# Kernel optimization log

Measured on AMD Instinct MI355X. Metric: run time of the kernel, lower is better.

Reference implementation:

```python
import jax, jax.numpy as jnp
import numpy as np

D_MODEL = 512
N_HEADS = 8
D_HEAD = D_MODEL // N_HEADS
SCALE = 1.0 / np.sqrt(D_MODEL).astype(np.float32)  # source divides by sqrt(d_model), not sqrt(d_head)


def setup_inputs() -> dict:
    key = jax.random.key(0)
    ks = jax.random.split(key, 9)
    B, S = 4, 2048
    std = 1.0 / np.sqrt(D_MODEL).astype(np.float32)
    x = jax.random.normal(ks[0], (B, S, D_MODEL), dtype=jnp.float32)
    Wq = jax.random.normal(ks[1], (D_MODEL, D_MODEL), dtype=jnp.float32) * std
    bq = jnp.zeros((D_MODEL,), jnp.float32)
    Wk = jax.random.normal(ks[2], (D_MODEL, D_MODEL), dtype=jnp.float32) * std
    bk = jnp.zeros((D_MODEL,), jnp.float32)
    Wv = jax.random.normal(ks[3], (D_MODEL, D_MODEL), dtype=jnp.float32) * std
    bv = jnp.zeros((D_MODEL,), jnp.float32)
    Wo = jax.random.normal(ks[4], (D_MODEL, D_MODEL), dtype=jnp.float32) * std
    bo = jnp.zeros((D_MODEL,), jnp.float32)
    return {"x": x, "Wq": Wq, "bq": bq, "Wk": Wk, "bk": bk,
            "Wv": Wv, "bv": bv, "Wo": Wo, "bo": bo}


def reference(x, Wq, bq, Wk, bk, Wv, bv, Wo, bo):
    B, S, _ = x.shape
    # projections -> [B, H, S, Dh]
    def split_heads(t):
        return t.reshape(B, S, N_HEADS, D_HEAD).transpose(0, 2, 1, 3)
    q = split_heads(x @ Wq + bq)
    k = split_heads(x @ Wk + bk)
    v = split_heads(x @ Wv + bv)
    # scores: [B, H, S, S], scaled by 1/sqrt(d_model) as in source
    scores = jnp.einsum('bhqd,bhkd->bhqk', q, k) * SCALE
    weights = jax.nn.softmax(scores, axis=-1)
    # dropout is identity at inference time
    att = jnp.einsum('bhqk,bhkd->bhqd', weights, v)
    att = att.transpose(0, 2, 1, 3).reshape(B, S, D_MODEL)
    return att @ Wo + bo
```

## Files before the change

kernel.cpp:

```cpp
#include <hip/hip_runtime.h>
#include <math.h>

#define BATCH   4
#define S_LEN   2048
#define DMODEL  512
#define NHEADS  8
#define DHEAD   64
#define M_TOT   8192
#define ATT_SCALE 0.04419417382415922f
#define QSCALE (ATT_SCALE * 1.44269504088896f)

using short8  = __attribute__((ext_vector_type(8))) short;
using short4v = __attribute__((ext_vector_type(4))) short;
using floatx4 = __attribute__((ext_vector_type(4))) float;

__device__ __forceinline__ ushort f2bf(float f) {
    union { float f; unsigned u; } x; x.f = f;
    unsigned u = x.u + 0x7FFFu + ((x.u >> 16) & 1u);
    return (ushort)(u >> 16);
}
__device__ __forceinline__ unsigned pk2(float a, float b) {
    return (unsigned)f2bf(a) | ((unsigned)f2bf(b) << 16);
}
__device__ __forceinline__ unsigned pkr2(float a, float b) {
    unsigned ua = __float_as_uint(a) + 0x8000u;
    unsigned ub = __float_as_uint(b) + 0x8000u;
    return __builtin_amdgcn_perm(ub, ua, 0x07060302u);
}

__global__ __launch_bounds__(256) void prep(
    const float* __restrict__ x,
    const float* __restrict__ Wq, const float* __restrict__ Wk,
    const float* __restrict__ Wv, const float* __restrict__ Wo,
    ushort* __restrict__ xb, ushort* __restrict__ WT)
{
    const int bid = blockIdx.x;
    if (bid < 4096) {
        const int i = (bid * 256 + threadIdx.x) * 4;
        float4 f = *(const float4*)(x + i);
        uint2 o; o.x = pk2(f.x, f.y); o.y = pk2(f.z, f.w);
        *(uint2*)(xb + i) = o;
    } else {
        const int rb = bid - 4096;
        const int p  = rb >> 6;
        const int rem = rb & 63;
        const int n  = (rem >> 5) * 256 + threadIdx.x;
        const int k0 = (rem & 31) * 16;
        const float* W = (p == 0) ? Wq : (p == 1) ? Wk : (p == 2) ? Wv : Wo;
        unsigned u[8];
        #pragma unroll
        for (int j = 0; j < 8; ++j) {
            float a = W[(k0 + 2 * j)     * DMODEL + n];
            float b = W[(k0 + 2 * j + 1) * DMODEL + n];
            u[j] = pk2(a, b);
        }
        ushort* dst = WT + ((size_t)p * DMODEL + n) * DMODEL + k0;
        *(uint4*)dst       = *(uint4*)&u[0];
        *(uint4*)(dst + 8) = *(uint4*)&u[4];
    }
}

__global__ __launch_bounds__(256, 4) void qkv_gemm(
    const ushort* __restrict__ xb, const ushort* __restrict__ WT,
    const float* __restrict__ bq, const float* __restrict__ bk, const float* __restrict__ bv,
    ushort* __restrict__ q, ushort* __restrict__ k, ushort* __restrict__ vT)
{
    __shared__ ushort SMEM[128 * 136];
    ushort (*A)[40] = (ushort(*)[40])SMEM;
    ushort (*B)[40] = (ushort(*)[40])(SMEM + 128 * 40);
    ushort (*CT)[136] = (ushort(*)[136])SMEM;

    const int tid = threadIdx.x;
    const int wv  = tid >> 6, lane = tid & 63, l16 = lane & 15, quad = lane >> 4;
    const int m0  = blockIdx.x * 128;
    const int ng0 = blockIdx.y * 128;
    const int p   = ng0 >> 9;
    const int n0  = ng0 & 511;
    const ushort* Wp  = WT + (size_t)p * DMODEL * DMODEL + (size_t)n0 * DMODEL;
    const float* bias = (p == 0) ? bq : (p == 1) ? bk : bv;
    const float scl   = (p == 0) ? QSCALE : 1.0f;

    const int wm = (wv & 1) * 64, wn = (wv >> 1) * 64;
    floatx4 acc[4][4] = {};
    const int ar = tid >> 1, ac = (tid & 1) * 16;

    uint4 pa0, pa1, pb0, pb1;
    pa0 = *(const uint4*)(xb + (size_t)(m0 + ar) * DMODEL + ac);
    pa1 = *(const uint4*)(xb + (size_t)(m0 + ar) * DMODEL + ac + 8);
    pb0 = *(const uint4*)(Wp + (size_t)ar * DMODEL + ac);
    pb1 = *(const uint4*)(Wp + (size_t)ar * DMODEL + ac + 8);

    for (int k0 = 0; k0 < DMODEL; k0 += 32) {
        *(uint4*)&A[ar][ac] = pa0; *(uint4*)&A[ar][ac + 8] = pa1;
        *(uint4*)&B[ar][ac] = pb0; *(uint4*)&B[ar][ac + 8] = pb1;
        __syncthreads();

        if (k0 + 32 < DMODEL) {
            pa0 = *(const uint4*)(xb + (size_t)(m0 + ar) * DMODEL + k0 + 32 + ac);
            pa1 = *(const uint4*)(xb + (size_t)(m0 + ar) * DMODEL + k0 + 32 + ac + 8);
            pb0 = *(const uint4*)(Wp + (size_t)ar * DMODEL + k0 + 32 + ac);
            pb1 = *(const uint4*)(Wp + (size_t)ar * DMODEL + k0 + 32 + ac + 8);
        }

        short8 af[4], bf[4];
        #pragma unroll
        for (int i = 0; i < 4; ++i) af[i] = *(const short8*)&A[wm + i * 16 + l16][quad * 8];
        #pragma unroll
        for (int c = 0; c < 4; ++c) bf[c] = *(const short8*)&B[wn + c * 16 + l16][quad * 8];
        #pragma unroll
        for (int i = 0; i < 4; ++i)
            #pragma unroll
            for (int c = 0; c < 4; ++c)
                acc[i][c] = __builtin_amdgcn_mfma_f32_16x16x32_bf16(af[i], bf[c], acc[i][c], 0, 0, 0);
        __syncthreads();
    }

    if (p < 2) {
        #pragma unroll
        for (int c = 0; c < 4; ++c) {
            const int n = n0 + wn + c * 16 + l16;
            const float bb = bias[n];
            const int h = n >> 6, dh = n & 63;
            #pragma unroll
            for (int i = 0; i < 4; ++i)
                #pragma unroll
                for (int r = 0; r < 4; ++r) {
                    const int m = m0 + wm + i * 16 + quad * 4 + r;
                    const int b = m >> 11, s = m & 2047;
                    const ushort val = f2bf((acc[i][c][r] + bb) * scl);
                    if (p == 0) q[((size_t)(b * NHEADS + h) * S_LEN + s) * DHEAD + dh] = val;
                    else        k[((size_t)(b * NHEADS + h) * S_LEN + s) * DHEAD + dh] = val;
                }
        }
    } else {
        #pragma unroll
        for (int c = 0; c < 4; ++c) {
            const int n = wn + c * 16 + l16;
            const float bb = bias[n0 + n];
            #pragma unroll
            for (int i = 0; i < 4; ++i) {
                uint2 o;
                o.x = pk2(acc[i][c][0] + bb, acc[i][c][1] + bb);
                o.y = pk2(acc[i][c][2] + bb, acc[i][c][3] + bb);
                *(uint2*)&CT[n][wm + i * 16 + quad * 4] = o;
            }
        }
        __syncthreads();
        const int n  = tid >> 1, mh = (tid & 1) * 64;
        const int gn = n0 + n;
        const int h  = gn >> 6, dh = gn & 63;
        const int b  = m0 >> 11, sb = (m0 & 2047) + mh;
        ushort* dst = vT + ((size_t)(b * NHEADS + h) * DHEAD + dh) * S_LEN + sb;
        #pragma unroll
        for (int j = 0; j < 8; ++j)
            *(uint4*)(dst + j * 8) = *(const uint4*)&CT[n][mh + j * 8];
    }
}

__global__ __launch_bounds__(256, 4) void attn(
    const ushort* __restrict__ Q, const ushort* __restrict__ K,
    const ushort* __restrict__ vT,
    ushort* __restrict__ att, const int KT)
{
    __shared__ ushort Klds[2][64][72];
    __shared__ ushort Vt[2][64][72];

    const int tid = threadIdx.x;
    const int wv  = tid >> 6, lane = tid & 63, l16 = lane & 15, quad = lane >> 4;
    const int q0  = blockIdx.x * 128;
    const int bh  = blockIdx.y;
    const ushort* Qh = Q  + (size_t)bh * S_LEN * DHEAD;
    const ushort* Kh = K  + (size_t)bh * S_LEN * DHEAD;
    const ushort* Vh = vT + (size_t)bh * DHEAD * S_LEN;

    short8 qf[2][2];
    #pragma unroll
    for (int ni = 0; ni < 2; ++ni) {
        const ushort* qrow = Qh + (size_t)(q0 + wv * 32 + ni * 16 + l16) * DHEAD;
        qf[0][ni] = *(const short8*)(qrow + quad * 8);
        qf[1][ni] = *(const short8*)(qrow + 32 + quad * 8);
    }

    floatx4 oacc[4][2] = {};
    float lsum[2] = {0.f, 0.f};

    const int srow = tid >> 2, sc0 = (tid & 3) * 16;
    uint4 ka, kb, va, vb;
    {
        const ushort* Ks = Kh + (size_t)srow * DHEAD + sc0;
        const ushort* Vs = Vh + (size_t)srow * S_LEN + sc0;
        ka = *(const uint4*)Ks; kb = *(const uint4*)(Ks + 8);
        va = *(const uint4*)Vs; vb = *(const uint4*)(Vs + 8);
    }

    for (int kt = 0; kt < KT; ++kt) {
        const int buf = kt & 1;
        *(uint4*)&Klds[buf][srow][sc0] = ka; *(uint4*)&Klds[buf][srow][sc0 + 8] = kb;
        *(uint4*)&Vt[buf][srow][sc0]   = va; *(uint4*)&Vt[buf][srow][sc0 + 8]   = vb;
        __syncthreads();

        if (kt + 1 < KT) {
            const ushort* Ks = Kh + (size_t)((kt + 1) * 64 + srow) * DHEAD + sc0;
            const ushort* Vs = Vh + (size_t)srow * S_LEN + (kt + 1) * 64 + sc0;
            ka = *(const uint4*)Ks; kb = *(const uint4*)(Ks + 8);
            va = *(const uint4*)Vs; vb = *(const uint4*)(Vs + 8);
        }

        #pragma unroll
        for (int mi = 0; mi < 4; ++mi) {
            floatx4 s0 = {}, s1 = {};
            #pragma unroll
            for (int s = 0; s < 2; ++s) {
                short8 kf = *(const short8*)&Klds[buf][mi * 16 + l16][s * 32 + quad * 8];
                s0 = __builtin_amdgcn_mfma_f32_16x16x32_bf16(kf, qf[s][0], s0, 0, 0, 0);
                s1 = __builtin_amdgcn_mfma_f32_16x16x32_bf16(kf, qf[s][1], s1, 0, 0, 0);
            }
            short4v vfr[4];
            #pragma unroll
            for (int c = 0; c < 4; ++c)
                vfr[c] = *(const short4v*)&Vt[buf][c * 16 + l16][mi * 16 + quad * 4];

            {
                const float p0 = __builtin_amdgcn_exp2f(s0[0]);
                const float p1 = __builtin_amdgcn_exp2f(s0[1]);
                const float p2 = __builtin_amdgcn_exp2f(s0[2]);
                const float p3 = __builtin_amdgcn_exp2f(s0[3]);
                lsum[0] += (p0 + p1) + (p2 + p3);
                uint2 o; o.x = pkr2(p0, p1); o.y = pkr2(p2, p3);
                short4v pf; *(uint2*)&pf = o;
                #pragma unroll
                for (int c = 0; c < 4; ++c)
                    oacc[c][0] = __builtin_amdgcn_mfma_f32_16x16x16bf16_1k(vfr[c], pf, oacc[c][0], 0, 0, 0);
            }
            {
                const float p0 = __builtin_amdgcn_exp2f(s1[0]);
                const float p1 = __builtin_amdgcn_exp2f(s1[1]);
                const float p2 = __builtin_amdgcn_exp2f(s1[2]);
                const float p3 = __builtin_amdgcn_exp2f(s1[3]);
                lsum[1] += (p0 + p1) + (p2 + p3);
                uint2 o; o.x = pkr2(p0, p1); o.y = pkr2(p2, p3);
                short4v pf; *(uint2*)&pf = o;
                #pragma unroll
                for (int c = 0; c < 4; ++c)
                    oacc[c][1] = __builtin_amdgcn_mfma_f32_16x16x16bf16_1k(vfr[c], pf, oacc[c][1], 0, 0, 0);
            }
        }
    }

    float rin[2];
    #pragma unroll
    for (int ni = 0; ni < 2; ++ni) {
        float t = lsum[ni];
        t += __shfl_xor(t, 16, 64);
        t += __shfl_xor(t, 32, 64);
        rin[ni] = 1.0f / t;
    }

    const int b = bh >> 3, h = bh & 7;
    #pragma unroll
    for (int ni = 0; ni < 2; ++ni) {
        const int qg = q0 + wv * 32 + ni * 16 + l16;
        ushort* orow = att + ((size_t)(b * S_LEN + qg)) * DMODEL + h * DHEAD + quad * 4;
        #pragma unroll
        for (int c = 0; c < 4; ++c) {
            uint2 o;
            o.x = pk2(oacc[c][ni][0] * rin[ni], oacc[c][ni][1] * rin[ni]);
            o.y = pk2(oacc[c][ni][2] * rin[ni], oacc[c][ni][3] * rin[ni]);
            *(uint2*)(orow + c * 16) = o;
        }
    }
}

__global__ __launch_bounds__(256, 4) void out_gemm(
    const ushort* __restrict__ att,
    const ushort* __restrict__ WoT, const float* __restrict__ bo,
    float* __restrict__ out)
{
    __shared__ ushort A[64][40];
    __shared__ ushort B[128][40];

    const int tid = threadIdx.x;
    const int wv  = tid >> 6, lane = tid & 63, l16 = lane & 15, quad = lane >> 4;
    const int m0 = blockIdx.x * 64;
    const int n0 = blockIdx.y * 128;

    const int ar = tid >> 2, ac = (tid & 3) * 8;
    const int br = tid >> 1, bc = (tid & 1) * 16;

    floatx4 acc[8] = {};

    for (int k0 = 0; k0 < DMODEL; k0 += 32) {
        *(uint4*)&A[ar][ac] = *(const uint4*)(att + (size_t)(m0 + ar) * DMODEL + k0 + ac);
        uint4 b0 = *(const uint4*)(WoT + (size_t)(n0 + br) * DMODEL + k0 + bc);
        uint4 b1 = *(const uint4*)(WoT + (size_t)(n0 + br) * DMODEL + k0 + bc + 8);
        *(uint4*)&B[br][bc] = b0; *(uint4*)&B[br][bc + 8] = b1;
        __syncthreads();

        short8 af = *(const short8*)&A[wv * 16 + l16][quad * 8];
        #pragma unroll
        for (int c = 0; c < 8; ++c) {
            short8 bf = *(const short8*)&B[c * 16 + l16][quad * 8];
            acc[c] = __builtin_amdgcn_mfma_f32_16x16x32_bf16(af, bf, acc[c], 0, 0, 0);
        }
        __syncthreads();
    }

    #pragma unroll
    for (int c = 0; c < 8; ++c) {
        const int n = n0 + c * 16 + l16;
        const float bb = bo[n];
        #pragma unroll
        for (int r = 0; r < 4; ++r) {
            const int m = m0 + wv * 16 + quad * 4 + r;
            out[(size_t)m * DMODEL + n] = acc[c][r] + bb;
        }
    }
}

extern "C" void kernel_launch(void* const* d_in, const int* in_sizes, int n_in,
                              void* d_out, int out_size, void* d_ws, size_t ws_size,
                              hipStream_t stream)
{
    const float* x  = (const float*)d_in[0];
    const float* Wq = (const float*)d_in[1];
    const float* bq = (const float*)d_in[2];
    const float* Wk = (const float*)d_in[3];
    const float* bk = (const float*)d_in[4];
    const float* Wv = (const float*)d_in[5];
    const float* bv = (const float*)d_in[6];
    const float* Wo = (const float*)d_in[7];
    const float* bo = (const float*)d_in[8];
    float* out = (float*)d_out;

    ushort* ws = (ushort*)d_ws;
    const size_t SZ = (size_t)M_TOT * DMODEL;
    ushort* xb  = ws;
    ushort* WT  = ws + SZ;
    ushort* q   = WT + 4 * (size_t)DMODEL * DMODEL;
    ushort* k   = q + SZ;
    ushort* vT  = k + SZ;
    ushort* att = vT + SZ;

    prep<<<4096 + 256, 256, 0, stream>>>(x, Wq, Wk, Wv, Wo, xb, WT);

    qkv_gemm<<<dim3(M_TOT / 128, 3 * DMODEL / 128), 256, 0, stream>>>(
        xb, WT, bq, bk, bv, q, k, vT);

    attn<<<dim3(S_LEN / 128, BATCH * NHEADS), 256, 0, stream>>>(
        q, k, vT, att, S_LEN / 64);

    out_gemm<<<dim3(M_TOT / 64, DMODEL / 128), 256, 0, stream>>>(
        att, WT + 3 * (size_t)DMODEL * DMODEL, bo, out);
}
```

Baseline: 174.2 us.

## Split key tiles across wave halves in attention and prefetch out-GEMM tiles

The attention kernel now uses 512-thread blocks covering 256 queries. Each wave handles 64 queries and half of each 64-key tile, so every K fragment loaded from LDS feeds four query sub-tiles instead of two, with s_setprio hints around the MFMA bursts. The two key-half partial outputs and row sums are combined through LDS at the end, which adds extra synchronisation and a reduction. The output GEMM also register-prefetches the next K-slice of A and B while computing the current one. The larger per-wave accumulator state raises register pressure, and the attention grid has half as many blocks.

```diff
diff --git a/kernel.cpp b/kernel.cpp
--- a/kernel.cpp
+++ b/kernel.cpp
@@ -157,117 +157,149 @@
     }
 }
 
-__global__ __launch_bounds__(256, 4) void attn(
+__global__ __launch_bounds__(512, 2) void attn(
     const ushort* __restrict__ Q, const ushort* __restrict__ K,
     const ushort* __restrict__ vT,
     ushort* __restrict__ att, const int KT)
 {
-    __shared__ ushort Klds[2][64][72];
-    __shared__ ushort Vt[2][64][72];
-
-    const int tid = threadIdx.x;
-    const int wv  = tid >> 6, lane = tid & 63, l16 = lane & 15, quad = lane >> 4;
-    const int q0  = blockIdx.x * 128;
-    const int bh  = blockIdx.y;
+    __shared__ ushort SMEM[18432];
+    ushort (*Klds)[64][72] = (ushort(*)[64][72])SMEM;
+    ushort (*Vt)[64][72]   = (ushort(*)[64][72])(SMEM + 9216);
+    float  (*Ored)[68]     = (float(*)[68])SMEM;
+    float*  Lred           = (float*)SMEM + 128 * 68;
+
+    const int tid  = threadIdx.x;
+    const int wv   = tid >> 6, lane = tid & 63, l16 = lane & 15, quad = lane >> 4;
+    const int qsub = wv & 3, khalf = wv >> 2;
+    const int q0   = blockIdx.x * 256;
+    const int bh   = blockIdx.y;
     const ushort* Qh = Q  + (size_t)bh * S_LEN * DHEAD;
     const ushort* Kh = K  + (size_t)bh * S_LEN * DHEAD;
     const ushort* Vh = vT + (size_t)bh * DHEAD * S_LEN;
 
-    short8 qf[2][2];
-    #pragma unroll
-    for (int ni = 0; ni < 2; ++ni) {
-        const ushort* qrow = Qh + (size_t)(q0 + wv * 32 + ni * 16 + l16) * DHEAD;
+    short8 qf[2][4];
+    #pragma unroll
+    for (int ni = 0; ni < 4; ++ni) {
+        const ushort* qrow = Qh + (size_t)(q0 + qsub * 64 + ni * 16 + l16) * DHEAD;
         qf[0][ni] = *(const short8*)(qrow + quad * 8);
         qf[1][ni] = *(const short8*)(qrow + 32 + quad * 8);
     }
 
-    floatx4 oacc[4][2] = {};
-    float lsum[2] = {0.f, 0.f};
-
-    const int srow = tid >> 2, sc0 = (tid & 3) * 16;
-    uint4 ka, kb, va, vb;
+    floatx4 oacc[4][4] = {};
+    float lsum[4] = {0.f, 0.f, 0.f, 0.f};
+
+    const int srow = tid >> 3, sc0 = (tid & 7) * 8;
+    uint4 ka, va;
     {
         const ushort* Ks = Kh + (size_t)srow * DHEAD + sc0;
         const ushort* Vs = Vh + (size_t)srow * S_LEN + sc0;
-        ka = *(const uint4*)Ks; kb = *(const uint4*)(Ks + 8);
-        va = *(const uint4*)Vs; vb = *(const uint4*)(Vs + 8);
+        ka = *(const uint4*)Ks; va = *(const uint4*)Vs;
     }
 
     for (int kt = 0; kt < KT; ++kt) {
         const int buf = kt & 1;
-        *(uint4*)&Klds[buf][srow][sc0] = ka; *(uint4*)&Klds[buf][srow][sc0 + 8] = kb;
-        *(uint4*)&Vt[buf][srow][sc0]   = va; *(uint4*)&Vt[buf][srow][sc0 + 8]   = vb;
+        *(uint4*)&Klds[buf][srow][sc0] = ka;
+        *(uint4*)&Vt[buf][srow][sc0]   = va;
         __syncthreads();
 
         if (kt + 1 < KT) {
             const ushort* Ks = Kh + (size_t)((kt + 1) * 64 + srow) * DHEAD + sc0;
             const ushort* Vs = Vh + (size_t)srow * S_LEN + (kt + 1) * 64 + sc0;
-            ka = *(const uint4*)Ks; kb = *(const uint4*)(Ks + 8);
-            va = *(const uint4*)Vs; vb = *(const uint4*)(Vs + 8);
-        }
-
-        #pragma unroll
-        for (int mi = 0; mi < 4; ++mi) {
-            floatx4 s0 = {}, s1 = {};
-            #pragma unroll
-            for (int s = 0; s < 2; ++s) {
-                short8 kf = *(const short8*)&Klds[buf][mi * 16 + l16][s * 32 + quad * 8];
-                s0 = __builtin_amdgcn_mfma_f32_16x16x32_bf16(kf, qf[s][0], s0, 0, 0, 0);
-                s1 = __builtin_amdgcn_mfma_f32_16x16x32_bf16(kf, qf[s][1], s1, 0, 0, 0);
-            }
+            ka = *(const uint4*)Ks; va = *(const uint4*)Vs;
+        }
+
+        #pragma unroll
+        for (int m2 = 0; m2 < 2; ++m2) {
+            const int mi = khalf * 2 + m2;
+            floatx4 sv[4] = {};
+            short8 kf0 = *(const short8*)&Klds[buf][mi * 16 + l16][quad * 8];
+            short8 kf1 = *(const short8*)&Klds[buf][mi * 16 + l16][32 + quad * 8];
+            __builtin_amdgcn_s_setprio(1);
+            #pragma unroll
+            for (int ni = 0; ni < 4; ++ni) {
+                sv[ni] = __builtin_amdgcn_mfma_f32_16x16x32_bf16(kf0, qf[0][ni], sv[ni], 0, 0, 0);
+                sv[ni] = __builtin_amdgcn_mfma_f32_16x16x32_bf16(kf1, qf[1][ni], sv[ni], 0, 0, 0);
+            }
+            __builtin_amdgcn_s_setprio(0);
             short4v vfr[4];
             #pragma unroll
             for (int c = 0; c < 4; ++c)
                 vfr[c] = *(const short4v*)&Vt[buf][c * 16 + l16][mi * 16 + quad * 4];
 
-            {
-                const float p0 = __builtin_amdgcn_exp2f(s0[0]);
-                const float p1 = __builtin_amdgcn_exp2f(s0[1]);
-                const float p2 = __builtin_amdgcn_exp2f(s0[2]);
-                const float p3 = __builtin_amdgcn_exp2f(s0[3]);
-                lsum[0] += (p0 + p1) + (p2 + p3);
+            #pragma unroll
+            for (int ni = 0; ni < 4; ++ni) {
+                const float p0 = __builtin_amdgcn_exp2f(sv[ni][0]);
+                const float p1 = __builtin_amdgcn_exp2f(sv[ni][1]);
+                const float p2 = __builtin_amdgcn_exp2f(sv[ni][2]);
+                const float p3 = __builtin_amdgcn_exp2f(sv[ni][3]);
+                lsum[ni] += (p0 + p1) + (p2 + p3);
                 uint2 o; o.x = pkr2(p0, p1); o.y = pkr2(p2, p3);
                 short4v pf; *(uint2*)&pf = o;
+                __builtin_amdgcn_s_setprio(1);
                 #pragma unroll
                 for (int c = 0; c < 4; ++c)
-                    oacc[c][0] = __builtin_amdgcn_mfma_f32_16x16x16bf16_1k(vfr[c], pf, oacc[c][0], 0, 0, 0);
-            }
-            {
-                const float p0 = __builtin_amdgcn_exp2f(s1[0]);
-                const float p1 = __builtin_amdgcn_exp2f(s1[1]);
-                const float p2 = __builtin_amdgcn_exp2f(s1[2]);
-                const float p3 = __builtin_amdgcn_exp2f(s1[3]);
-                lsum[1] += (p0 + p1) + (p2 + p3);
-                uint2 o; o.x = pkr2(p0, p1); o.y = pkr2(p2, p3);
-                short4v pf; *(uint2*)&pf = o;
-                #pragma unroll
-                for (int c = 0; c < 4; ++c)
-                    oacc[c][1] = __builtin_amdgcn_mfma_f32_16x16x16bf16_1k(vfr[c], pf, oacc[c][1], 0, 0, 0);
-            }
-        }
-    }
-
-    float rin[2];
-    #pragma unroll
-    for (int ni = 0; ni < 2; ++ni) {
+                    oacc[c][ni] = __builtin_amdgcn_mfma_f32_16x16x16bf16_1k(vfr[c], pf, oacc[c][ni], 0, 0, 0);
+                __builtin_amdgcn_s_setprio(0);
+            }
+        }
+    }
+
+    float tot[4];
+    #pragma unroll
+    for (int ni = 0; ni < 4; ++ni) {
         float t = lsum[ni];
         t += __shfl_xor(t, 16, 64);
         t += __shfl_xor(t, 32, 64);
-        rin[ni] = 1.0f / t;
+        tot[ni] = t;
+    }
+
+    __syncthreads();
+    if (quad == 0) {
+        #pragma unroll
+        for (int ni = 0; ni < 4; ++ni)
+            Lred[khalf * 256 + qsub * 64 + ni * 16 + l16] = tot[ni];
+    }
+    __syncthreads();
+    float rin[4];
+    #pragma unroll
+    for (int ni = 0; ni < 4; ++ni) {
+        const int qq = qsub * 64 + ni * 16 + l16;
+        rin[ni] = 1.0f / (Lred[qq] + Lred[256 + qq]);
     }
 
     const int b = bh >> 3, h = bh & 7;
     #pragma unroll
-    for (int ni = 0; ni < 2; ++ni) {
-        const int qg = q0 + wv * 32 + ni * 16 + l16;
-        ushort* orow = att + ((size_t)(b * S_LEN + qg)) * DMODEL + h * DHEAD + quad * 4;
-        #pragma unroll
-        for (int c = 0; c < 4; ++c) {
-            uint2 o;
-            o.x = pk2(oacc[c][ni][0] * rin[ni], oacc[c][ni][1] * rin[ni]);
-            o.y = pk2(oacc[c][ni][2] * rin[ni], oacc[c][ni][3] * rin[ni]);
-            *(uint2*)(orow + c * 16) = o;
-        }
+    for (int ph = 0; ph < 2; ++ph) {
+        if (khalf == 1 && (qsub >> 1) == ph) {
+            #pragma unroll
+            for (int ni = 0; ni < 4; ++ni) {
+                const int row = (qsub & 1) * 64 + ni * 16 + l16;
+                #pragma unroll
+                for (int c = 0; c < 4; ++c) {
+                    float4 o = { oacc[c][ni][0], oacc[c][ni][1],
+                                 oacc[c][ni][2], oacc[c][ni][3] };
+                    *(float4*)&Ored[row][c * 16 + quad * 4] = o;
+                }
+            }
+        }
+        __syncthreads();
+        if (khalf == 0 && (qsub >> 1) == ph) {
+            #pragma unroll
+            for (int ni = 0; ni < 4; ++ni) {
+                const int row = (qsub & 1) * 64 + ni * 16 + l16;
+                const int qg  = q0 + qsub * 64 + ni * 16 + l16;
+                ushort* orow = att + ((size_t)(b * S_LEN + qg)) * DMODEL + h * DHEAD + quad * 4;
+                #pragma unroll
+                for (int c = 0; c < 4; ++c) {
+                    float4 u = *(const float4*)&Ored[row][c * 16 + quad * 4];
+                    uint2 o;
+                    o.x = pk2((oacc[c][ni][0] + u.x) * rin[ni], (oacc[c][ni][1] + u.y) * rin[ni]);
+                    o.y = pk2((oacc[c][ni][2] + u.z) * rin[ni], (oacc[c][ni][3] + u.w) * rin[ni]);
+                    *(uint2*)(orow + c * 16) = o;
+                }
+            }
+        }
+        __syncthreads();
     }
 }
 
@@ -289,12 +321,21 @@
 
     floatx4 acc[8] = {};
 
+    uint4 pa, pb0, pb1;
+    pa  = *(const uint4*)(att + (size_t)(m0 + ar) * DMODEL + ac);
+    pb0 = *(const uint4*)(WoT + (size_t)(n0 + br) * DMODEL + bc);
+    pb1 = *(const uint4*)(WoT + (size_t)(n0 + br) * DMODEL + bc + 8);
+
     for (int k0 = 0; k0 < DMODEL; k0 += 32) {
-        *(uint4*)&A[ar][ac] = *(const uint4*)(att + (size_t)(m0 + ar) * DMODEL + k0 + ac);
-        uint4 b0 = *(const uint4*)(WoT + (size_t)(n0 + br) * DMODEL + k0 + bc);
-        uint4 b1 = *(const uint4*)(WoT + (size_t)(n0 + br) * DMODEL + k0 + bc + 8);
-        *(uint4*)&B[br][bc] = b0; *(uint4*)&B[br][bc + 8] = b1;
-        __syncthreads();
+        *(uint4*)&A[ar][ac] = pa;
+        *(uint4*)&B[br][bc] = pb0; *(uint4*)&B[br][bc + 8] = pb1;
+        __syncthreads();
+
+        if (k0 + 32 < DMODEL) {
+            pa  = *(const uint4*)(att + (size_t)(m0 + ar) * DMODEL + k0 + 32 + ac);
+            pb0 = *(const uint4*)(WoT + (size_t)(n0 + br) * DMODEL + k0 + 32 + bc);
+            pb1 = *(const uint4*)(WoT + (size_t)(n0 + br) * DMODEL + k0 + 32 + bc + 8);
+        }
 
         short8 af = *(const short8*)&A[wv * 16 + l16][quad * 8];
         #pragma unroll
@@ -346,7 +387,7 @@
     qkv_gemm<<<dim3(M_TOT / 128, 3 * DMODEL / 128), 256, 0, stream>>>(
         xb, WT, bq, bk, bv, q, k, vT);
 
-    attn<<<dim3(S_LEN / 128, BATCH * NHEADS), 256, 0, stream>>>(
+    attn<<<dim3(S_LEN / 256, BATCH * NHEADS), 512, 0, stream>>>(
         q, k, vT, att, S_LEN / 64);
 
     out_gemm<<<dim3(M_TOT / 64, DMODEL / 128), 256, 0, stream>>>(
```

Measured after the change: 165.2 us. 5.2% less time.
